# Optimization experiments

Hardware: AMD Instinct MI355X
Metric: run time of the kernel (lower is better)

## Reference

```python
import jax, jax.numpy as jnp
from jax import lax
import numpy as np

K = 32          # PyG radius_graph default max_num_neighbors
NEG = -1e9      # mask fill for max-aggregation


def _gather(a, i):  # a [N,C], i [...,] int -> a[i]
    return a[i]


def radius_knn(pos, r):
    # pos [B,N,3] -> (idx [B,N,K], valid [B,N,K]) nearest-K within radius r, self excluded
    sq = jnp.sum(pos * pos, -1)                                   # [B,N]
    d2 = sq[:, :, None] + sq[:, None, :] - 2.0 * jnp.einsum('bnc,bmc->bnm', pos, pos)
    N = pos.shape[1]
    d2 = d2 + jnp.eye(N, dtype=pos.dtype) * 1e9                    # exclude self-loops
    neg, idx = lax.top_k(-d2, K)
    valid = (-neg) <= r * r
    return idx, valid


def fps(pos, n):
    # iterative farthest point sampling, deterministic start at index 0; pos [B,N,3] -> idx [B,n]
    def one(p):
        mind0 = jnp.sum((p - p[0]) ** 2, -1)
        def step(mind, _):
            i = jnp.argmax(mind)
            nd = jnp.sum((p - p[i]) ** 2, -1)
            return jnp.minimum(mind, nd), i
        _, idxs = lax.scan(step, mind0, None, length=n - 1)
        return jnp.concatenate([jnp.zeros((1,), jnp.int32), idxs.astype(jnp.int32)])
    return jax.vmap(one)(pos)


def point_conv(x, pos, idx, valid, W1, b1, W2, b2):
    # PyG PointNetConv: msg = local_nn(concat(x_j, pos_j - pos_i)), max-aggregate
    g = jax.vmap(_gather)
    rel = g(pos, idx) - pos[:, :, None, :]                         # [B,N,K,3]
    feat = rel if x is None else jnp.concatenate([g(x, idx), rel], -1)
    h = jax.nn.relu(feat @ W1 + b1) @ W2 + b2                      # [B,N,K,C]
    h = jnp.where(valid[..., None], h, NEG)
    return jnp.max(h, axis=2)                                      # [B,N,C]


def _forward(pos, W1a, b1a, W1b, b1b, W2a, b2a, W2b, b2b, W3a, b3a, W3b, b3b,
             Wc1, bc1, Wc2, bc2, Wc3, bc3, Wd1, bd1, Wd2, bd2):
    take = jax.vmap(_gather)
    B, N, _ = pos.shape
    idx, v = radius_knn(pos, 0.2)
    x = jax.nn.relu(point_conv(None, pos, idx, v, W1a, b1a, W1b, b1b))
    fi = fps(pos, N // 2)
    x, pos = take(x, fi), take(pos, fi)
    idx, v = radius_knn(pos, 0.4)
    x = jax.nn.relu(point_conv(x, pos, idx, v, W2a, b2a, W2b, b2b))
    fi = fps(pos, N // 8)
    x, pos = take(x, fi), take(pos, fi)
    idx, v = radius_knn(pos, 1.0)
    x = jax.nn.relu(point_conv(x, pos, idx, v, W3a, b3a, W3b, b3b))
    feat = jnp.max(x, axis=1)                                      # global max pool [B,256]
    h = jax.nn.relu(feat @ Wc1 + bc1)
    h = jax.nn.relu(h @ Wc2 + bc2)                                 # dropout is identity in eval
    logits = h @ Wc3 + bc3
    h2 = jax.nn.relu(feat @ Wd1 + bd1)
    d = h2 @ Wd2 + bd2
    return jax.nn.log_softmax(logits, axis=-1), jax.nn.log_softmax(d, axis=-1)


def setup_inputs() -> dict:
    key = jax.random.key(0)
    ks = jax.random.split(key, 32)
    def lin(k, fin, fout):
        kw, kb = jax.random.split(k)
        s = 1.0 / np.sqrt(fin)
        return (jax.random.uniform(kw, (fin, fout), jnp.float32, -s, s),
                jax.random.uniform(kb, (fout,), jnp.float32, -s, s))
    inp = {'pos': jax.random.uniform(ks[0], (8, 4096, 3), jnp.float32)}
    names = [('W1a','b1a',3,64),('W1b','b1b',64,64),('W2a','b2a',67,128),('W2b','b2b',128,128),
             ('W3a','b3a',131,256),('W3b','b3b',256,256),('Wc1','bc1',256,256),('Wc2','bc2',256,256),
             ('Wc3','bc3',256,40),('Wd1','bd1',256,256),('Wd2','bd2',256,2)]
    for i, (wn, bn, fin, fout) in enumerate(names):
        W, b = lin(ks[i + 1], fin, fout)
        inp[wn], inp[bn] = W, b
    return inp


def reference(pos, W1a, b1a, W1b, b1b, W2a, b2a, W2b, b2b, W3a, b3a, W3b, b3b,
              Wc1, bc1, Wc2, bc2, Wc3, bc3, Wd1, bd1, Wd2, bd2):
    return _forward(pos, W1a, b1a, W1b, b1b, W2a, b2a, W2b, b2b, W3a, b3a, W3b, b3b,
                    Wc1, bc1, Wc2, bc2, Wc3, bc3, Wd1, bd1, Wd2, bd2)
```

## Files before the change

kernel.cpp:

```cpp
#include <hip/hip_runtime.h>


#define NB 8

__device__ __forceinline__ unsigned obits(float f) {
  unsigned u = __float_as_uint(f);
  return (u & 0x80000000u) ? ~u : (u | 0x80000000u);
}

static constexpr int CAND = 1024;

template<int CTRL>
__device__ __forceinline__ unsigned long long dpp_max_step(unsigned long long v) {
  const int lo = (int)(unsigned)(v & 0xffffffffull);
  const int hi = (int)(unsigned)(v >> 32);
  const unsigned nlo = (unsigned)__builtin_amdgcn_update_dpp(lo, lo, CTRL, 0xf, 0xf, false);
  const unsigned nhi = (unsigned)__builtin_amdgcn_update_dpp(hi, hi, CTRL, 0xf, 0xf, false);
  const unsigned long long nv = ((unsigned long long)nhi << 32) | nlo;
  return (nv > v) ? nv : v;
}

__device__ __forceinline__ unsigned wave_iscan_add(unsigned x) {
  x += (unsigned)__builtin_amdgcn_update_dpp(0, (int)x, 0x111, 0xf, 0xf, true);
  x += (unsigned)__builtin_amdgcn_update_dpp(0, (int)x, 0x112, 0xf, 0xf, true);
  x += (unsigned)__builtin_amdgcn_update_dpp(0, (int)x, 0x114, 0xf, 0xf, true);
  x += (unsigned)__builtin_amdgcn_update_dpp(0, (int)x, 0x118, 0xf, 0xf, true);
  x += (unsigned)__builtin_amdgcn_update_dpp(0, (int)x, 0x142, 0xa, 0xf, true);
  x += (unsigned)__builtin_amdgcn_update_dpp(0, (int)x, 0x143, 0xc, 0xf, true);
  return x;
}

__device__ __forceinline__ unsigned long long u64max(unsigned long long a,
                                                    unsigned long long b) {
  return (b > a) ? b : a;
}

__device__ __forceinline__ void set_wave_prio_hi() {
#if __has_builtin(__builtin_amdgcn_s_setprio)
  __builtin_amdgcn_s_setprio(3);
#endif
}

template<int N, int NOUT, int T>
__device__ __forceinline__ void fps_body(char* sm, const float* __restrict__ pb,
                                         int* __restrict__ fi, int b) {
  constexpr int P = N / T;
  constexpr int NW = T / 64;
  constexpr int CELLS = (N >= 4096) ? 512 : 256;
  constexpr int CZB = (CELLS == 512) ? 3 : 2;
  constexpr int CH = NOUT;
  constexpr int NCHUNK = N / CH;
  static_assert(CH % P == 0 && N % CH == 0, "chunking");
  int4* sPosI = (int4*)sm;
  int*  sfi   = (int*)(sm + (size_t)N * 16);
  unsigned long long* sKey =
      (unsigned long long*)(sm + (size_t)N * 16 + NOUT * 4);
  unsigned* hist = (unsigned*)(sm + (size_t)N * 16 + NOUT * 4 + 128);
  int* sOrd = sfi;
  const int tid = threadIdx.x, wid = tid >> 6, lane = tid & 63;
  set_wave_prio_hi();

  for (int t = tid; t < N; t += T) {
    sPosI[t] = make_int4((int)(pb[3*t]   * 8388608.f),
                         (int)(pb[3*t+1] * 8388608.f),
                         (int)(pb[3*t+2] * 8388608.f), 0);
  }
  for (int c = tid; c < CELLS; c += T) hist[c] = 0u;
  __syncthreads();

  unsigned myc[P];
#pragma unroll
  for (int r = 0; r < P; r++) {
    const int t = tid + r * T;
    const int4 p4 = sPosI[t];
    const unsigned cell = (((unsigned)p4.x >> 20) << (3 + CZB)) |
                          (((unsigned)p4.y >> 20) << CZB) |
                          ((unsigned)p4.z >> (23 - CZB));
    myc[r] = cell;
    atomicAdd(&hist[cell], 1u);
  }
  __syncthreads();

  {
    unsigned* sPart = (unsigned*)sKey;
    unsigned v = (tid < CELLS) ? hist[tid] : 0u;
    const unsigned isc = wave_iscan_add(v);
    if (lane == 63) sPart[wid] = isc;
    __syncthreads();
    unsigned offs = 0;
#pragma unroll
    for (int w2 = 0; w2 < NW; w2++) offs += (w2 < wid) ? sPart[w2] : 0u;
    if (tid < CELLS) hist[tid] = offs + isc - v;
    __syncthreads();
  }

  int myslot[P];
#pragma unroll
  for (int r = 0; r < P; r++) myslot[r] = (int)atomicAdd(&hist[myc[r]], 1u);

  int ex[P], ey[P], ez[P]; unsigned einv[P];
  for (int pc = 0; pc < NCHUNK; pc++) {
    __syncthreads();
#pragma unroll
    for (int r = 0; r < P; r++) {
      const int s = myslot[r];
      if (s >= pc * CH && s < (pc + 1) * CH) sOrd[s - pc * CH] = tid + r * T;
    }
    __syncthreads();
    if ((tid * P) / CH == pc) {
#pragma unroll
      for (int e = 0; e < P; e++) {
        const int o = sOrd[tid * P + e - pc * CH];
        const int4 p4 = sPosI[o];
        ex[e] = p4.x; ey[e] = p4.y; ez[e] = p4.z;
        einv[e] = (unsigned)(4095 - o);
      }
    }
  }
  __syncthreads();

  int lox = ex[0], hix = ex[0], loy = ey[0], hiy = ey[0], loz = ez[0], hiz = ez[0];
#pragma unroll
  for (int e = 1; e < P; e++) {
    lox = min(lox, ex[e]); hix = max(hix, ex[e]);
    loy = min(loy, ey[e]); hiy = max(hiy, ey[e]);
    loz = min(loz, ez[e]); hiz = max(hiz, ez[e]);
  }

  const int4 p0 = sPosI[0];
  unsigned long long mind[P];
  unsigned long long bv;
  {
    unsigned long long tv[P];
#pragma unroll
    for (int e = 0; e < P; e++) {
      const long long dx = ex[e] - p0.x, dy = ey[e] - p0.y, dz = ez[e] - p0.z;
      const unsigned long long d2 =
          (unsigned long long)(dx * dx + dy * dy + dz * dz);
      const unsigned long long k = (d2 << 12) | einv[e];
      mind[e] = k; tv[e] = k;
    }
#pragma unroll
    for (int s = 1; s < P; s <<= 1)
#pragma unroll
      for (int e = 0; e + s < P; e += 2 * s)
        if (tv[e + s] > tv[e]) tv[e] = tv[e + s];
    bv = tv[0];
  }
  if (tid == 0) sfi[0] = 0;

  for (int t = 1; t < NOUT; t++) {
    unsigned long long v = bv;
    v = dpp_max_step<0x111>(v);
    v = dpp_max_step<0x112>(v);
    v = dpp_max_step<0x114>(v);
    v = dpp_max_step<0x118>(v);
    v = dpp_max_step<0x142>(v);
    v = dpp_max_step<0x143>(v);
    const int pp = t & 1;
    if (lane == 63) sKey[pp * NW + wid] = v;
    __syncthreads();
    unsigned long long best;
    if (NW == 8) {
      unsigned long long k0 = sKey[pp*8+0], k1 = sKey[pp*8+1],
                         k2 = sKey[pp*8+2], k3 = sKey[pp*8+3],
                         k4 = sKey[pp*8+4], k5 = sKey[pp*8+5],
                         k6 = sKey[pp*8+6], k7 = sKey[pp*8+7];
      k0 = u64max(k0, k1); k2 = u64max(k2, k3);
      k4 = u64max(k4, k5); k6 = u64max(k6, k7);
      k0 = u64max(k0, k2); k4 = u64max(k4, k6);
      best = u64max(k0, k4);
    } else {
      unsigned long long k0 = sKey[pp*NW+0];
#pragma unroll
      for (int w2 = 1; w2 < NW; w2++) k0 = u64max(k0, sKey[pp*NW+w2]);
      best = k0;
    }
    const int ii = 4095 - (int)(best & 0xFFFull);
    if (tid == 0) sfi[t] = ii;
    const int4 wc = sPosI[ii];

    const int ax = max(max(lox - wc.x, wc.x - hix), 0);
    const int ay = max(max(loy - wc.y, wc.y - hiy), 0);
    const int az = max(max(loz - wc.z, wc.z - hiz), 0);
    const unsigned long long lb =
        (unsigned long long)ax * (unsigned long long)ax +
        (unsigned long long)ay * (unsigned long long)ay +
        (unsigned long long)az * (unsigned long long)az;
    if (lb < (bv >> 12)) {
      unsigned long long tv[P];
#pragma unroll
      for (int e = 0; e < P; e++) {
        const long long dx = ex[e] - wc.x, dy = ey[e] - wc.y, dz = ez[e] - wc.z;
        const unsigned long long nd =
            (unsigned long long)(dx * dx + dy * dy + dz * dz);
        const unsigned long long nk = (nd << 12) | einv[e];
        unsigned long long mk = mind[e];
        mk = (nk < mk) ? nk : mk;
        mind[e] = mk;
        tv[e] = mk;
      }
#pragma unroll
      for (int s = 1; s < P; s <<= 1)
#pragma unroll
        for (int e = 0; e + s < P; e += 2 * s)
          if (tv[e + s] > tv[e]) tv[e] = tv[e + s];
      bv = tv[0];
    }
  }
  __syncthreads();
  for (int t = tid; t < NOUT; t += T) fi[(size_t)b * NOUT + t] = sfi[t];
}

template<int N, int H, int C, bool HASX, bool FOLDMAX, int T>
__device__ __forceinline__ void knnconv_body(
    char* sm, const float* __restrict__ pb, int b, int i,
    const float* __restrict__ U, const float* __restrict__ Wrel,
    const float* __restrict__ b1, const float* __restrict__ W2,
    const float* __restrict__ b2, float* __restrict__ out, double rr) {
  constexpr int HCHUNK = (C == 64) ? 64 : (C == 128 ? 32 : 16);
  constexpr int STR = HCHUNK + 4;
  constexpr int NW = T / 64;
  constexpr int EPK = 32 / NW;
  constexpr int BPT = 2048 / T;
  constexpr int KNNFRONT = N * 8 + 13312;
  constexpr int CONVFRONT = 32 * H * 4 + C * STR * 4 + NW * C * 4;
  constexpr int FRONT = (KNNFRONT > CONVFRONT) ? KNNFRONT : CONVFRONT;
  double*   d2s     = (double*)sm;
  unsigned* hist    = (unsigned*)(sm + N * 8);
  int*      candIdx = (int*)(sm + N * 8 + 8192);
  unsigned* sWT     = (unsigned*)(sm + N * 8 + 12288);
  float* h1s  = (float*)sm;
  float* sW2T = (float*)(sm + 32 * H * 4);
  float* sRed = (float*)(sm + 32 * H * 4 + C * STR * 4);
  int*   snbr = (int*)(sm + FRONT);
  float* rel  = (float*)(sm + FRONT + 128);
  int*   pcnt = (int*)(sm + FRONT + 128 + 384);
  int*   pbin = pcnt + 1;
  const int tid = threadIdx.x;

  const double xi = pb[3*i], yi = pb[3*i+1], zi = pb[3*i+2];
  const double si = (xi*xi + yi*yi) + zi*zi;
  for (int t = tid; t < 2048; t += T) hist[t] = 0u;
  if (tid == 0) *pcnt = 0;
  __syncthreads();
  for (int j = tid; j < N; j += T) {
    double xj = pb[3*j], yj = pb[3*j+1], zj = pb[3*j+2];
    double sj = (xj*xj + yj*yj) + zj*zj;
    double dt = (xi*xj + yi*yj) + zi*zj;
    double d2 = (si + sj) - 2.0*dt;
    if (j == i) d2 += 1e9;
    d2s[j] = d2;
    atomicAdd(&hist[obits((float)d2) >> 21], 1u);
  }
  __syncthreads();
  unsigned lsum = 0;
  const int base = tid * BPT;
#pragma unroll
  for (int q = 0; q < BPT; q++) lsum += hist[base + q];
  const unsigned isc = wave_iscan_add(lsum);
  if ((tid & 63) == 63) sWT[tid >> 6] = isc;
  __syncthreads();
  {
    const int wid = tid >> 6;
    unsigned offs = 0;
#pragma unroll
    for (int w2 = 0; w2 < NW; w2++) offs += (w2 < wid) ? sWT[w2] : 0u;
    const unsigned incl = isc + offs, excl = incl - lsum;
    if (excl < 32u && incl >= 32u) {
      unsigned c = excl;
      for (int q = 0; q < BPT; q++) {
        c += hist[base + q];
        if (c >= 32u) { *pbin = base + q; break; }
      }
    }
  }
  __syncthreads();
  const int binT = *pbin;
  for (int j = tid; j < N; j += T) {
    if ((int)(obits((float)d2s[j]) >> 21) <= binT) {
      int p = atomicAdd(pcnt, 1);
      if (p < CAND) candIdx[p] = j;
    }
  }
  __syncthreads();
  const int M = min(*pcnt, CAND);
  for (int c = tid; c < M; c += T) {
    const int j = candIdx[c];
    const double d = d2s[j];
    int rank = 0;
    for (int e = 0; e < M; e++) {
      const int j2 = candIdx[e];
      const double de = d2s[j2];
      rank += (de < d || (de == d && j2 < j)) ? 1 : 0;
    }
    if (rank < 32) snbr[rank] = (d <= rr) ? j : -1;
  }
  __syncthreads();

  if (tid < 32) {
    const int j = snbr[tid];
    float rx = 0.f, ry = 0.f, rz = 0.f;
    if (j >= 0) {
      rx = pb[3*j]   - pb[3*i];
      ry = pb[3*j+1] - pb[3*i+1];
      rz = pb[3*j+2] - pb[3*i+2];
    }
    rel[tid*3+0] = rx; rel[tid*3+1] = ry; rel[tid*3+2] = rz;
  }
  __syncthreads();

  constexpr int QPK = H / 4;
  for (int qi = tid; qi < 32 * QPK; qi += T) {
    const int k = qi / QPK, h0 = (qi - k * QPK) * 4;
    const int j = snbr[k];
    float4 v = make_float4(0.f, 0.f, 0.f, 0.f);
    if (j >= 0) {
      float4 a = HASX ? *(const float4*)&U[((size_t)b * N + j) * H + h0]
                      : *(const float4*)&b1[h0];
      const float rx = rel[k*3], ry = rel[k*3+1], rz = rel[k*3+2];
      const float4 w0 = *(const float4*)&Wrel[h0];
      const float4 w1 = *(const float4*)&Wrel[H + h0];
      const float4 w2 = *(const float4*)&Wrel[2 * H + h0];
      a.x += rx * w0.x + ry * w1.x + rz * w2.x;
      a.y += rx * w0.y + ry * w1.y + rz * w2.y;
      a.z += rx * w0.z + ry * w1.z + rz * w2.z;
      a.w += rx * w0.w + ry * w1.w + rz * w2.w;
      v = make_float4(fmaxf(a.x, 0.f), fmaxf(a.y, 0.f),
                      fmaxf(a.z, 0.f), fmaxf(a.w, 0.f));
    }
    *(float4*)&h1s[k * H + h0] = v;
  }
  const int cc = tid & 63;
  const int kk = tid >> 6;
  constexpr int CC = C / 64;
  float acc[EPK][CC];
#pragma unroll
  for (int e = 0; e < EPK; e++)
#pragma unroll
    for (int q = 0; q < CC; q++) acc[e][q] = 0.f;
  for (int hc = 0; hc < H; hc += HCHUNK) {
    __syncthreads();
    for (int idx = tid; idx < HCHUNK * C; idx += T) {
      const int hh = idx / C, c = idx - hh * C;
      sW2T[c * STR + hh] = W2[(size_t)(hc + hh) * C + c];
    }
    __syncthreads();
    for (int hh0 = 0; hh0 < HCHUNK; hh0 += 4) {
      float4 wv[CC];
#pragma unroll
      for (int q = 0; q < CC; q++)
        wv[q] = *(const float4*)&sW2T[(cc + q * 64) * STR + hh0];
#pragma unroll
      for (int e = 0; e < EPK; e++) {
        const float4 hv = *(const float4*)&h1s[(kk + e * NW) * H + hc + hh0];
#pragma unroll
        for (int q = 0; q < CC; q++) {
          acc[e][q] += hv.x * wv[q].x;
          acc[e][q] += hv.y * wv[q].y;
          acc[e][q] += hv.z * wv[q].z;
          acc[e][q] += hv.w * wv[q].w;
        }
      }
    }
  }
  float m[CC];
#pragma unroll
  for (int q = 0; q < CC; q++) m[q] = -1e9f;
#pragma unroll
  for (int e = 0; e < EPK; e++) {
    if (snbr[kk + e * NW] >= 0) {
#pragma unroll
      for (int q = 0; q < CC; q++) m[q] = fmaxf(m[q], acc[e][q]);
    }
  }
#pragma unroll
  for (int q = 0; q < CC; q++) sRed[kk * C + cc + q * 64] = m[q];
  __syncthreads();
  if (kk == 0) {
#pragma unroll
    for (int q = 0; q < CC; q++) {
      const int c = cc + q * 64;
      float mm = sRed[c];
#pragma unroll
      for (int w2 = 1; w2 < NW; w2++) mm = fmaxf(mm, sRed[w2 * C + c]);
      const float o = (mm > -5e8f) ? (mm + b2[c]) : -1e9f;
      const float r = fmaxf(o, 0.f);
      if (FOLDMAX) {
        atomicMax((int*)&out[b * C + c], __float_as_int(r));
      } else {
        out[((size_t)b * N + i) * C + c] = r;
      }
    }
  }
}

template<int N, int NOUT, int H, int C, bool HASX, int SMSIZE>
__device__ __forceinline__ void stage_fused_impl(
    const float* pos, double rr, int* fi, const float* U, const float* Wrel,
    const float* b1, const float* W2, const float* b2, float* out, char* sm) {
  if (blockIdx.x < NB) {
    fps_body<N, NOUT, 512>(sm, pos + (size_t)blockIdx.x * N * 3, fi, blockIdx.x);
  } else {
    const int row = blockIdx.x - NB;
    const int b = row / N;
    const int i = row - b * N;
    knnconv_body<N, H, C, HASX, false, 512>(sm, pos + (size_t)b * N * 3, b, i,
                                            U, Wrel, b1, W2, b2, out, rr);
  }
}

__global__ __launch_bounds__(512, 2)
void stage1_kernel(const float* __restrict__ pos, double rr, int* __restrict__ fi,
                   const float* __restrict__ Wrel, const float* __restrict__ b1,
                   const float* __restrict__ W2, const float* __restrict__ b2,
                   float* __restrict__ out) {
  __shared__ __align__(16) char sm[75904];
  stage_fused_impl<4096, 2048, 64, 64, false, 75904>(
      pos, rr, fi, nullptr, Wrel, b1, W2, b2, out, sm);
}

__global__ __launch_bounds__(512, 2)
void stage2_kernel(const float* __restrict__ pos, double rr, int* __restrict__ fi,
                   const float* __restrict__ U, const float* __restrict__ Wrel,
                   const float* __restrict__ b1, const float* __restrict__ W2,
                   const float* __restrict__ b2, float* __restrict__ out) {
  __shared__ __align__(16) char sm[39440];
  stage_fused_impl<2048, 512, 128, 128, true, 39440>(
      pos, rr, fi, U, Wrel, b1, W2, b2, out, sm);
}

__global__ __launch_bounds__(512)
void stage3_kernel(const float* __restrict__ pos, double rr,
                   const float* __restrict__ U, const float* __restrict__ Wrel,
                   const float* __restrict__ b1, const float* __restrict__ W2,
                   const float* __restrict__ b2, float* __restrict__ feat) {
  __shared__ __align__(16) char sm[61968];
  const int b = blockIdx.x / 512;
  const int i = blockIdx.x - b * 512;
  knnconv_body<512, 256, 256, true, true, 512>(sm, pos + (size_t)b * 512 * 3,
                                               b, i, U, Wrel, b1, W2, b2,
                                               feat, rr);
}

template<int CIN, int HH>
__global__ __launch_bounds__(HH)
void gp_kernel(const float* __restrict__ X, const float* __restrict__ posPrev,
               const int* __restrict__ fi, int Nprev, int M,
               const float* __restrict__ W, const float* __restrict__ bias,
               float* __restrict__ U, float* __restrict__ posDst) {
  const int row = blockIdx.x;
  const int b = row / M;
  const int tid = threadIdx.x;
  const int j = fi[row];
  __shared__ float sx[CIN];
  if (tid < CIN) sx[tid] = X[((size_t)b * Nprev + j) * CIN + tid];
  if (tid < 3) posDst[(size_t)row * 3 + tid] = posPrev[((size_t)b * Nprev + j) * 3 + tid];
  __syncthreads();
  float a = bias[tid];
  for (int f = 0; f < CIN; f++) a = fmaf(sx[f], W[f * HH + tid], a);
  U[(size_t)row * HH + tid] = a;
}

__global__ __launch_bounds__(256) void head_kernel(
    const float* __restrict__ feat,
    const float* __restrict__ Wc1, const float* __restrict__ bc1,
    const float* __restrict__ Wc2, const float* __restrict__ bc2,
    const float* __restrict__ Wc3, const float* __restrict__ bc3,
    const float* __restrict__ Wd1, const float* __restrict__ bd1,
    const float* __restrict__ Wd2, const float* __restrict__ bd2,
    float* __restrict__ out) {
  const int b = blockIdx.x, tid = threadIdx.x;
  __shared__ float sf[256], sh[256], sh2[256], shd[256], sl[48];
  sf[tid] = feat[b * 256 + tid];
  __syncthreads();
  float a = bc1[tid], ad = bd1[tid];
  for (int f = 0; f < 256; f++) {
    const float fv = sf[f];
    a  = fmaf(fv, Wc1[f * 256 + tid], a);
    ad = fmaf(fv, Wd1[f * 256 + tid], ad);
  }
  sh[tid] = fmaxf(a, 0.f);
  shd[tid] = fmaxf(ad, 0.f);
  __syncthreads();
  float a2 = bc2[tid];
  for (int f = 0; f < 256; f++) a2 = fmaf(sh[f], Wc2[f * 256 + tid], a2);
  sh2[tid] = fmaxf(a2, 0.f);
  __syncthreads();
  if (tid < 40) {
    float l = bc3[tid];
    for (int f = 0; f < 256; f++) l = fmaf(sh2[f], Wc3[f * 40 + tid], l);
    sl[tid] = l;
  }
  if (tid >= 64 && tid < 66) {
    const int q = tid - 64;
    float l = bd2[q];
    for (int f = 0; f < 256; f++) l = fmaf(shd[f], Wd2[f * 2 + q], l);
    sl[40 + q] = l;
  }
  __syncthreads();
  if (tid == 0) {
    float m0 = sl[0];
    for (int q = 1; q < 40; q++) m0 = fmaxf(m0, sl[q]);
    float s = 0.f;
    for (int q = 0; q < 40; q++) s += expf(sl[q] - m0);
    const float ls = logf(s);
    for (int q = 0; q < 40; q++) out[b * 40 + q] = sl[q] - m0 - ls;
    const float m1 = fmaxf(sl[40], sl[41]);
    const float s1 = expf(sl[40] - m1) + expf(sl[41] - m1);
    const float ls1 = logf(s1);
    out[320 + b * 2 + 0] = sl[40] - m1 - ls1;
    out[320 + b * 2 + 1] = sl[41] - m1 - ls1;
  }
}

extern "C" void kernel_launch(void* const* d_in, const int* in_sizes, int n_in,
                              void* d_out, int out_size, void* d_ws, size_t ws_size,
                              hipStream_t stream) {
  (void)in_sizes; (void)n_in; (void)out_size; (void)ws_size;
  const float* pos = (const float*)d_in[0];
  const float* W1a = (const float*)d_in[1];  const float* b1a = (const float*)d_in[2];
  const float* W1b = (const float*)d_in[3];  const float* b1b = (const float*)d_in[4];
  const float* W2a = (const float*)d_in[5];  const float* b2a = (const float*)d_in[6];
  const float* W2b = (const float*)d_in[7];  const float* b2b = (const float*)d_in[8];
  const float* W3a = (const float*)d_in[9];  const float* b3a = (const float*)d_in[10];
  const float* W3b = (const float*)d_in[11]; const float* b3b = (const float*)d_in[12];
  const float* Wc1 = (const float*)d_in[13]; const float* bc1 = (const float*)d_in[14];
  const float* Wc2 = (const float*)d_in[15]; const float* bc2 = (const float*)d_in[16];
  const float* Wc3 = (const float*)d_in[17]; const float* bc3 = (const float*)d_in[18];
  const float* Wd1 = (const float*)d_in[19]; const float* bd1 = (const float*)d_in[20];
  const float* Wd2 = (const float*)d_in[21]; const float* bd2 = (const float*)d_in[22];
  float* out = (float*)d_out;

  char* w = (char*)d_ws;
  auto alloc = [&](size_t bytes) -> void* {
    void* p = (void*)w;
    w += (bytes + 255) & ~(size_t)255;
    return p;
  };
  int*   fi1  = (int*)  alloc((size_t)NB*2048*4);
  float* x1   = (float*)alloc((size_t)NB*4096*64*4);
  float* pos2 = (float*)alloc((size_t)NB*2048*3*4);
  float* U2   = (float*)alloc((size_t)NB*2048*128*4);
  float* x2   = (float*)alloc((size_t)NB*2048*128*4);
  int*   fi2  = (int*)  alloc((size_t)NB*512*4);
  float* pos3 = (float*)alloc((size_t)NB*512*3*4);
  float* U3   = (float*)alloc((size_t)NB*512*256*4);
  float* feat = (float*)alloc((size_t)NB*256*4);

  hipMemsetAsync(feat, 0, (size_t)NB * 256 * 4, stream);

  stage1_kernel<<<NB + NB * 4096, 512, 0, stream>>>(
      pos, 0.2 * 0.2, fi1, W1a, b1a, W1b, b1b, x1);

  gp_kernel<64, 128><<<NB * 2048, 128, 0, stream>>>(
      x1, pos, fi1, 4096, 2048, W2a, b2a, U2, pos2);

  stage2_kernel<<<NB + NB * 2048, 512, 0, stream>>>(
      pos2, 0.4 * 0.4, fi2, U2, W2a + (size_t)64 * 128, b2a, W2b, b2b, x2);

  gp_kernel<128, 256><<<NB * 512, 256, 0, stream>>>(
      x2, pos2, fi2, 2048, 512, W3a, b3a, U3, pos3);

  stage3_kernel<<<NB * 512, 512, 0, stream>>>(
      pos3, 1.0, U3, W3a + (size_t)128 * 256, b3a, W3b, b3b, feat);

  head_kernel<<<NB, 256, 0, stream>>>(feat, Wc1, bc1, Wc2, bc2, Wc3, bc3,
                                      Wd1, bd1, Wd2, bd2, out);
}
```

Measured before the change: 2.358 ms.

## Use Morton-ordered cells and per-wave-column bounding boxes to prune FPS updates

Points are now binned by a 3D Morton code over an 8x8x8 grid, and each wave takes P contiguous 64-point groups (one point per lane per slot) rather than each thread taking P consecutive points. Bounding boxes are computed per wave-wide column through DPP min/max reductions and read back from shared memory. A ballot then skips distance updates for whole columns whose box cannot beat the current global best distance, so the pruning works at wave granularity and removes divergence. The cost is a larger setup phase and a hardcoded 8-wave reduction path, which drops the generic NW fallback.

```diff
diff --git a/kernel.cpp b/kernel.cpp
--- a/kernel.cpp
+++ b/kernel.cpp
@@ -30,6 +30,27 @@
   return x;
 }
 
+__device__ __forceinline__ int wave_red_imax(int v) {
+  int n;
+  n = __builtin_amdgcn_update_dpp(v, v, 0x111, 0xf, 0xf, false); v = max(v, n);
+  n = __builtin_amdgcn_update_dpp(v, v, 0x112, 0xf, 0xf, false); v = max(v, n);
+  n = __builtin_amdgcn_update_dpp(v, v, 0x114, 0xf, 0xf, false); v = max(v, n);
+  n = __builtin_amdgcn_update_dpp(v, v, 0x118, 0xf, 0xf, false); v = max(v, n);
+  n = __builtin_amdgcn_update_dpp(v, v, 0x142, 0xf, 0xf, false); v = max(v, n);
+  n = __builtin_amdgcn_update_dpp(v, v, 0x143, 0xf, 0xf, false); v = max(v, n);
+  return v;
+}
+__device__ __forceinline__ int wave_red_imin(int v) {
+  int n;
+  n = __builtin_amdgcn_update_dpp(v, v, 0x111, 0xf, 0xf, false); v = min(v, n);
+  n = __builtin_amdgcn_update_dpp(v, v, 0x112, 0xf, 0xf, false); v = min(v, n);
+  n = __builtin_amdgcn_update_dpp(v, v, 0x114, 0xf, 0xf, false); v = min(v, n);
+  n = __builtin_amdgcn_update_dpp(v, v, 0x118, 0xf, 0xf, false); v = min(v, n);
+  n = __builtin_amdgcn_update_dpp(v, v, 0x142, 0xf, 0xf, false); v = min(v, n);
+  n = __builtin_amdgcn_update_dpp(v, v, 0x143, 0xf, 0xf, false); v = min(v, n);
+  return v;
+}
+
 __device__ __forceinline__ unsigned long long u64max(unsigned long long a,
                                                     unsigned long long b) {
   return (b > a) ? b : a;
@@ -39,6 +60,13 @@
 #if __has_builtin(__builtin_amdgcn_s_setprio)
   __builtin_amdgcn_s_setprio(3);
 #endif
+}
+
+__device__ __forceinline__ unsigned morton3_8(unsigned cx, unsigned cy, unsigned cz) {
+  unsigned m = ((cx & 1u) << 2) | ((cy & 1u) << 1) | (cz & 1u);
+  m |= ((cx & 2u) << 4) | ((cy & 2u) << 3) | ((cz & 2u) << 2);
+  m |= ((cx & 4u) << 6) | ((cy & 4u) << 5) | ((cz & 4u) << 4);
+  return m;
 }
 
 template<int N, int NOUT, int T>
@@ -46,16 +74,17 @@
                                          int* __restrict__ fi, int b) {
   constexpr int P = N / T;
   constexpr int NW = T / 64;
-  constexpr int CELLS = (N >= 4096) ? 512 : 256;
-  constexpr int CZB = (CELLS == 512) ? 3 : 2;
+  constexpr int WSLOTS = 64 * P;
+  constexpr int CELLS = 512;
   constexpr int CH = NOUT;
   constexpr int NCHUNK = N / CH;
-  static_assert(CH % P == 0 && N % CH == 0, "chunking");
+  static_assert(CH % WSLOTS == 0 && N % CH == 0, "chunking");
   int4* sPosI = (int4*)sm;
   int*  sfi   = (int*)(sm + (size_t)N * 16);
   unsigned long long* sKey =
       (unsigned long long*)(sm + (size_t)N * 16 + NOUT * 4);
   unsigned* hist = (unsigned*)(sm + (size_t)N * 16 + NOUT * 4 + 128);
+  int* sBB  = (int*)hist;
   int* sOrd = sfi;
   const int tid = threadIdx.x, wid = tid >> 6, lane = tid & 63;
   set_wave_prio_hi();
@@ -73,9 +102,9 @@
   for (int r = 0; r < P; r++) {
     const int t = tid + r * T;
     const int4 p4 = sPosI[t];
-    const unsigned cell = (((unsigned)p4.x >> 20) << (3 + CZB)) |
-                          (((unsigned)p4.y >> 20) << CZB) |
-                          ((unsigned)p4.z >> (23 - CZB));
+    const unsigned cell = morton3_8((unsigned)p4.x >> 20,
+                                    (unsigned)p4.y >> 20,
+                                    (unsigned)p4.z >> 20);
     myc[r] = cell;
     atomicAdd(&hist[cell], 1u);
   }
@@ -99,6 +128,7 @@
   for (int r = 0; r < P; r++) myslot[r] = (int)atomicAdd(&hist[myc[r]], 1u);
 
   int ex[P], ey[P], ez[P]; unsigned einv[P];
+  const int wbase = wid * WSLOTS;
   for (int pc = 0; pc < NCHUNK; pc++) {
     __syncthreads();
 #pragma unroll
@@ -107,10 +137,10 @@
       if (s >= pc * CH && s < (pc + 1) * CH) sOrd[s - pc * CH] = tid + r * T;
     }
     __syncthreads();
-    if ((tid * P) / CH == pc) {
+    if (wbase / CH == pc) {
 #pragma unroll
       for (int e = 0; e < P; e++) {
-        const int o = sOrd[tid * P + e - pc * CH];
+        const int o = sOrd[wbase + e * 64 + lane - pc * CH];
         const int4 p4 = sPosI[o];
         ex[e] = p4.x; ey[e] = p4.y; ez[e] = p4.z;
         einv[e] = (unsigned)(4095 - o);
@@ -119,12 +149,25 @@
   }
   __syncthreads();
 
-  int lox = ex[0], hix = ex[0], loy = ey[0], hiy = ey[0], loz = ez[0], hiz = ez[0];
-#pragma unroll
-  for (int e = 1; e < P; e++) {
-    lox = min(lox, ex[e]); hix = max(hix, ex[e]);
-    loy = min(loy, ey[e]); hiy = max(hiy, ey[e]);
-    loz = min(loz, ez[e]); hiz = max(hiz, ez[e]);
+  {
+#pragma unroll
+    for (int e = 0; e < P; e++) {
+      const int mnx = wave_red_imin(ex[e]), mxx = wave_red_imax(ex[e]);
+      const int mny = wave_red_imin(ey[e]), mxy = wave_red_imax(ey[e]);
+      const int mnz = wave_red_imin(ez[e]), mxz = wave_red_imax(ez[e]);
+      if (lane == 63) {
+        int* q = &sBB[(wid * P + e) * 6];
+        q[0] = mnx; q[1] = mxx; q[2] = mny; q[3] = mxy; q[4] = mnz; q[5] = mxz;
+      }
+    }
+  }
+  __syncthreads();
+  int clox, chix, cloy, chiy, cloz, chiz;
+  {
+    const int col = wid * P + (lane & (P - 1));
+    clox = sBB[col*6+0]; chix = sBB[col*6+1];
+    cloy = sBB[col*6+2]; chiy = sBB[col*6+3];
+    cloz = sBB[col*6+4]; chiz = sBB[col*6+5];
   }
 
   const int4 p0 = sPosI[0];
@@ -161,7 +204,7 @@
     if (lane == 63) sKey[pp * NW + wid] = v;
     __syncthreads();
     unsigned long long best;
-    if (NW == 8) {
+    {
       unsigned long long k0 = sKey[pp*8+0], k1 = sKey[pp*8+1],
                          k2 = sKey[pp*8+2], k3 = sKey[pp*8+3],
                          k4 = sKey[pp*8+4], k5 = sKey[pp*8+5],
@@ -170,36 +213,34 @@
       k4 = u64max(k4, k5); k6 = u64max(k6, k7);
       k0 = u64max(k0, k2); k4 = u64max(k4, k6);
       best = u64max(k0, k4);
-    } else {
-      unsigned long long k0 = sKey[pp*NW+0];
-#pragma unroll
-      for (int w2 = 1; w2 < NW; w2++) k0 = u64max(k0, sKey[pp*NW+w2]);
-      best = k0;
     }
     const int ii = 4095 - (int)(best & 0xFFFull);
     if (tid == 0) sfi[t] = ii;
     const int4 wc = sPosI[ii];
-
-    const int ax = max(max(lox - wc.x, wc.x - hix), 0);
-    const int ay = max(max(loy - wc.y, wc.y - hiy), 0);
-    const int az = max(max(loz - wc.z, wc.z - hiz), 0);
+    const unsigned long long bd2 = best >> 12;
+
+    const int ax = max(max(clox - wc.x, wc.x - chix), 0);
+    const int ay = max(max(cloy - wc.y, wc.y - chiy), 0);
+    const int az = max(max(cloz - wc.z, wc.z - chiz), 0);
     const unsigned long long lb =
         (unsigned long long)ax * (unsigned long long)ax +
         (unsigned long long)ay * (unsigned long long)ay +
         (unsigned long long)az * (unsigned long long)az;
-    if (lb < (bv >> 12)) {
+    const unsigned long long m = __ballot((lane < P) && (lb < bd2));
+    if (m != 0ull) {
+#pragma unroll
+      for (int e = 0; e < P; e++) {
+        if (m & (1ull << e)) {
+          const long long dx = ex[e] - wc.x, dy = ey[e] - wc.y, dz = ez[e] - wc.z;
+          const unsigned long long nd =
+              (unsigned long long)(dx * dx + dy * dy + dz * dz);
+          const unsigned long long nk = (nd << 12) | einv[e];
+          if (nk < mind[e]) mind[e] = nk;
+        }
+      }
       unsigned long long tv[P];
 #pragma unroll
-      for (int e = 0; e < P; e++) {
-        const long long dx = ex[e] - wc.x, dy = ey[e] - wc.y, dz = ez[e] - wc.z;
-        const unsigned long long nd =
-            (unsigned long long)(dx * dx + dy * dy + dz * dz);
-        const unsigned long long nk = (nd << 12) | einv[e];
-        unsigned long long mk = mind[e];
-        mk = (nk < mk) ? nk : mk;
-        mind[e] = mk;
-        tv[e] = mk;
-      }
+      for (int e = 0; e < P; e++) tv[e] = mind[e];
 #pragma unroll
       for (int s = 1; s < P; s <<= 1)
 #pragma unroll
```

Result: slower. 2.674 ms (+13.4%).
